# Kernel tuning notes

Hardware: AMD Instinct MI355X
Metric: run time of the kernel (lower is better)

The kernel has to match this reference:

```python
import jax, jax.numpy as jnp
import numpy as np

N_NODES = 40000
EMB = 256
NHEADS = 2
HEAD = EMB // NHEADS
NLAYERS = 4
NGNN = 2
LN_EPS = 1e-5
LEAKY = 0.01


def setup_inputs() -> dict:
    key = jax.random.key(0)
    ks = iter(jax.random.split(key, 40))
    nrm = lambda shape, s=0.05: jax.random.normal(next(ks), shape, dtype=jnp.float32) * s
    inp = {
        'feat0': nrm((20000, 512), 1.0),
        'feat1': nrm((20000, 512), 1.0),
        'fc_w0': nrm((256, 512)), 'fc_b0': jnp.zeros((256,), jnp.float32),
        'fc_w1': nrm((256, 512)), 'fc_b1': jnp.zeros((256,), jnp.float32),
        'gcn_w': nrm((NGNN, 256, 256)),
        'edge_src': jax.random.randint(next(ks), (640000,), 0, N_NODES),
        'edge_dst': jax.random.randint(next(ks), (640000,), 0, N_NODES),
        'dg_seqs': jax.random.randint(next(ks), (1024, 64), 0, N_NODES),
        'pt_seqs': jax.random.randint(next(ks), (1024, 64), 0, N_NODES),
        'type_emb': nrm((4, 4), 1.0),
        'node_type': jax.random.randint(next(ks), (N_NODES,), 0, 4),
        'gt_wl': nrm((8, 256, 256)), 'gt_wr': nrm((8, 256, 256)),
        'gt_al': nrm((8, 1, HEAD)), 'gt_ar': nrm((8, 1, HEAD)),
        'gt_wf': nrm((8, 256, 256)),
        'ln_g': jnp.ones((8, 256), jnp.float32), 'ln_b': jnp.zeros((8, 256), jnp.float32),
        'proj_d_w': nrm((2, 256, 256)), 'proj_d_b': jnp.zeros((2, 256), jnp.float32),
        'proj_p_w': nrm((2, 256, 256)), 'proj_p_b': jnp.zeros((2, 256), jnp.float32),
        'ml_w1': nrm((256, 512)), 'ml_b1': jnp.zeros((256,), jnp.float32),
        'ml_w2': nrm((128, 256)), 'ml_b2': jnp.zeros((128,), jnp.float32),
        'ml_w3': nrm((1, 128)), 'ml_b3': jnp.zeros((1,), jnp.float32),
    }
    return inp


def _layernorm(x, g, b):
    m = x.mean(-1, keepdims=True)
    v = ((x - m) ** 2).mean(-1, keepdims=True)
    return (x - m) * jax.lax.rsqrt(v + LN_EPS) * g + b


def _leaky(x):
    return jnp.where(x >= 0, x, LEAKY * x)


def _agt_layer(h, wl, wr, al, ar, wf, g, b):
    # h: [B, L, EMB]; additive (GAT-style) attention, temper = 1.0
    B, L, _ = h.shape
    fl = (h @ wl.T).reshape(B, L, NHEADS, HEAD).transpose(0, 2, 1, 3)  # [B,H,L,hd]
    fr = (h @ wr.T).reshape(B, L, NHEADS, HEAD).transpose(0, 2, 1, 3)
    sl = _leaky(fl) @ al.T                     # [B,H,L,1]
    sr = _leaky(fr) @ ar.T                     # [B,H,L,1]
    score = jax.nn.softmax(sl + sr.transpose(0, 1, 3, 2), axis=-1)  # [B,H,L,L]
    ctx = score @ fr                           # [B,H,L,hd]
    h_sa = ctx.transpose(0, 2, 1, 3).reshape(B, L, EMB)
    return _layernorm(h + h_sa @ wf.T, g, b)


def _gcn(gh, W, src, dst):
    # DGL GraphConv norm='both', allow_zero_in_degree, activation=relu
    ones = jnp.ones(src.shape[0], gh.dtype)
    deg_out = jnp.clip(jax.ops.segment_sum(ones, src, num_segments=N_NODES), 1.0)
    deg_in = jnp.clip(jax.ops.segment_sum(ones, dst, num_segments=N_NODES), 1.0)
    x = gh * (deg_out ** -0.5)[:, None]
    x = x @ W
    agg = jax.ops.segment_sum(x[src], dst, num_segments=N_NODES)
    return jax.nn.relu(agg * (deg_in ** -0.5)[:, None])


def reference(feat0, feat1, fc_w0, fc_b0, fc_w1, fc_b1, gcn_w, edge_src, edge_dst,
              dg_seqs, pt_seqs, type_emb, node_type, gt_wl, gt_wr, gt_al, gt_ar,
              gt_wf, ln_g, ln_b, proj_d_w, proj_d_b, proj_p_w, proj_p_b,
              ml_w1, ml_b1, ml_w2, ml_b2, ml_w3, ml_b3):
    # per-type input projections, concatenated along node dim
    h0 = feat0 @ fc_w0.T + fc_b0
    h1 = feat1 @ fc_w1.T + fc_b1
    gh = jnp.concatenate([h0, h1], axis=0)  # [N, EMB]
    r = type_emb[node_type]                 # computed but unused downstream (faithful)
    for layer in range(NGNN):
        gh = _gcn(gh, gcn_w[layer], edge_src, edge_dst)
    # graph transformer per node type (dropout = identity in eval)
    embs = []
    for t, seqs in ((0, dg_seqs), (1, pt_seqs)):
        h = gh[seqs]                        # [B, L, EMB]
        _ = r[seqs]
        for l in range(NLAYERS):
            i = t * NLAYERS + l
            h = _agt_layer(h, gt_wl[i], gt_wr[i], gt_al[i], gt_ar[i], gt_wf[i], ln_g[i], ln_b[i])
        embs.append(h[:, 0, :])
    dg_emb, pt_emb = embs
    # Proj heads: linear -> elu -> linear
    dg_emb = jax.nn.elu(dg_emb @ proj_d_w[0].T + proj_d_b[0]) @ proj_d_w[1].T + proj_d_b[1]
    pt_emb = jax.nn.elu(pt_emb @ proj_p_w[0].T + proj_p_b[0]) @ proj_p_w[1].T + proj_p_b[1]
    # Predict MLP on concat
    x = jnp.concatenate([dg_emb, pt_emb], axis=1)  # [B, 512]
    x = jax.nn.relu(x @ ml_w1.T + ml_b1)
    x = jax.nn.relu(x @ ml_w2.T + ml_b2)
    out = jax.nn.sigmoid(x @ ml_w3.T + ml_b3)
    return out.reshape(x.shape[0])
```

## Files before the change

### kernel.cpp

```cpp
#include <hip/hip_runtime.h>
#include <hip/hip_bf16.h>
#include <math.h>

typedef unsigned int u32;
typedef unsigned short u16;
typedef __attribute__((ext_vector_type(8))) short bf16x8;
typedef __attribute__((ext_vector_type(4))) float f32x4;

__device__ __forceinline__ float b2f(u16 u) { union { u32 i; float f; } c; c.i = ((u32)u) << 16; return c.f; }
__device__ __forceinline__ u16 f2b(float f) { __hip_bfloat16 h = __float2bfloat16(f); u16 r; __builtin_memcpy(&r, &h, 2); return r; }
__device__ __forceinline__ float b2f_lo(u32 w) { union { u32 i; float f; } c; c.i = w << 16; return c.f; }
__device__ __forceinline__ float b2f_hi(u32 w) { union { u32 i; float f; } c; c.i = w & 0xffff0000u; return c.f; }
__device__ __forceinline__ u32 pk2(float a, float b) { return (u32)f2b(a) | ((u32)f2b(b) << 16); }

__device__ __forceinline__ float wave_sum(float v) {
    #pragma unroll
    for (int off = 32; off > 0; off >>= 1) v += __shfl_xor(v, off, 64);
    return v;
}
__device__ __forceinline__ float wave_max(float v) {
    #pragma unroll
    for (int off = 32; off > 0; off >>= 1) v = fmaxf(v, __shfl_xor(v, off, 64));
    return v;
}

template<bool AF32>
__global__ __launch_bounds__(512) void mfma_gemm_kernel(
    const void* __restrict__ Av, const u16* __restrict__ B,
    const float* __restrict__ bias, const float* __restrict__ rowscale,
    u16* __restrict__ Cb, int M, int N, int K,
    const void* __restrict__ Av1, const u16* __restrict__ B1,
    const float* __restrict__ bias1, u16* __restrict__ Cb1)
{
    if (blockIdx.z) { Av = Av1; B = B1; bias = bias1; Cb = Cb1; }
    __shared__ u16 lds[2 * 128 * 64];
    const int tid = threadIdx.x;
    const int wid = tid >> 6, lane = tid & 63;
    const int wr = wid >> 1, wc = wid & 1;
    const int m0 = blockIdx.y * 128, n0 = blockIdx.x * 128;

    f32x4 acc[2][4] = {};

    const int rsub = lane >> 3;
    const int cbyte = (lane & 7) << 4;
    const int swz_st = cbyte ^ (rsub << 4);

    for (int k0 = 0; k0 < K; k0 += 64) {
        #pragma unroll
        for (int cc = 0; cc < 4; ++cc) {
            int c = wid * 4 + cc;
            int buf = c >> 4;
            int row_in = ((c & 15) << 3) + rsub;
            int lim = buf ? N : M;
            int row_g = (buf ? n0 : m0) + row_in;
            if (row_g >= lim) row_g = lim - 1;
            if (buf == 0 && AF32) {
                const float* src = (const float*)Av + (size_t)row_g * K + k0 + (cbyte >> 1);
                float4 v0 = *(const float4*)src;
                float4 v1 = *(const float4*)(src + 4);
                uint4 pk;
                pk.x = pk2(v0.x, v0.y); pk.y = pk2(v0.z, v0.w);
                pk.z = pk2(v1.x, v1.y); pk.w = pk2(v1.z, v1.w);
                *(uint4*)((char*)lds + row_in * 128 + swz_st) = pk;
            } else {
                const u16* srcb = (buf ? B : (const u16*)Av) + (size_t)row_g * K + k0 + (cbyte >> 1);
                f32x4 v = *(const f32x4*)srcb;
                *(f32x4*)((char*)lds + buf * 16384 + row_in * 128 + swz_st) = v;
            }
        }
        __syncthreads();
        #pragma unroll
        for (int ks = 0; ks < 2; ++ks) {
            const int off = (ks * 64 + ((lane >> 4) << 4)) ^ ((lane & 7) << 4);
            const int ra = lane & 15;
            bf16x8 af[2], bfr[4];
            #pragma unroll
            for (int i = 0; i < 2; ++i)
                af[i] = *(bf16x8*)((char*)lds + (wr * 32 + i * 16 + ra) * 128 + off);
            #pragma unroll
            for (int j = 0; j < 4; ++j)
                bfr[j] = *(bf16x8*)((char*)lds + 16384 + (wc * 64 + j * 16 + ra) * 128 + off);
            #pragma unroll
            for (int i = 0; i < 2; ++i)
                #pragma unroll
                for (int j = 0; j < 4; ++j)
                    acc[i][j] = __builtin_amdgcn_mfma_f32_16x16x32_bf16(af[i], bfr[j], acc[i][j], 0, 0, 0);
        }
        __syncthreads();
    }

    const int cr = lane >> 4, ccol = lane & 15;
    #pragma unroll
    for (int i = 0; i < 2; ++i) {
        #pragma unroll
        for (int j = 0; j < 4; ++j) {
            int colg = n0 + wc * 64 + j * 16 + ccol;
            if (colg >= N) continue;
            float badd = bias ? bias[colg] : 0.f;
            #pragma unroll
            for (int reg = 0; reg < 4; ++reg) {
                int rowg = m0 + wr * 32 + i * 16 + cr * 4 + reg;
                if (rowg >= M) continue;
                float v = acc[i][j][reg] + badd;
                if (rowscale) v *= rowscale[rowg];
                Cb[(size_t)rowg * N + colg] = f2b(v);
            }
        }
    }
}

__global__ __launch_bounds__(512, 4) void fused_transformer_kernel(
    const float* __restrict__ gh, const int* __restrict__ dg_seqs,
    const int* __restrict__ pt_seqs,
    const u16* __restrict__ wrN,
    const u32* __restrict__ wfT2,
    const float* __restrict__ ar,
    const float* __restrict__ lng, const float* __restrict__ lnb,
    float* __restrict__ embT)
{
    __shared__ u16 ldsA[64 * 256];
    __shared__ float sPart[8][64];
    __shared__ float pbuf[2][64];
    __shared__ float ctxS[256];
    __shared__ float uS2[2][256];

    const int tid = threadIdx.x;
    const int bx = blockIdx.x;
    const int t = bx >> 10, s = bx & 1023;
    const int r = tid >> 3, o8 = tid & 7;
    const int wid = tid >> 6, lane = tid & 63;
    const int hd = wid >> 2;
    const int g4 = lane >> 4, cl = lane & 15;

    const int* seqs = t ? pt_seqs : dg_seqs;

    float4 y[8];
    {
        int node = seqs[s * 64 + r];
        const float* src = gh + (size_t)node * 256 + o8 * 32;
        #pragma unroll
        for (int v = 0; v < 8; ++v) y[v] = *(const float4*)(src + v * 4);
    }

    for (int l = 0; l < 4; ++l) {
        const int li = t * 4 + l;
        {
            const int c = o8 >> 1, gb = (o8 & 1) * 4;
            #pragma unroll
            for (int gg = 0; gg < 4; ++gg) {
                float4 a = y[2 * gg], b = y[2 * gg + 1];
                uint4 pk;
                pk.x = pk2(a.x, a.y); pk.y = pk2(a.z, a.w);
                pk.z = pk2(b.x, b.y); pk.w = pk2(b.z, b.w);
                int g = gb + gg;
                *(uint4*)((char*)ldsA + c * 8192 + r * 128 + ((g << 4) ^ ((r & 7) << 4))) = pk;
            }
        }
        __syncthreads();

        f32x4 acc[4][2] = {};
        {
            const u16* wrl = wrN + (size_t)li * 65536;
            const int ra = lane & 15;
            #pragma unroll
            for (int kc = 0; kc < 8; ++kc) {
                const int c = kc >> 1, ks = kc & 1;
                const int off = (ks * 64 + ((lane >> 4) << 4)) ^ ((lane & 7) << 4);
                bf16x8 af[4], bfr[2];
                #pragma unroll
                for (int i = 0; i < 4; ++i)
                    af[i] = *(bf16x8*)((char*)ldsA + c * 8192 + (i * 16 + ra) * 128 + off);
                #pragma unroll
                for (int j = 0; j < 2; ++j)
                    bfr[j] = *(const bf16x8*)(wrl + ((size_t)((wid * 2 + j) * 8 + kc) << 9) + lane * 8);
                #pragma unroll
                for (int i = 0; i < 4; ++i)
                    #pragma unroll
                    for (int j = 0; j < 2; ++j)
                        acc[i][j] = __builtin_amdgcn_mfma_f32_16x16x32_bf16(af[i], bfr[j], acc[i][j], 0, 0, 0);
            }
        }

        {
            const float* arl = ar + li * 128;
            float arj[2];
            #pragma unroll
            for (int j = 0; j < 2; ++j) arj[j] = arl[(wid & 3) * 32 + j * 16 + cl];
            #pragma unroll
            for (int i = 0; i < 4; ++i)
                #pragma unroll
                for (int reg = 0; reg < 4; ++reg) {
                    float sc;
                    {
                        float x0 = acc[i][0][reg], x1 = acc[i][1][reg];
                        sc = (x0 >= 0.f ? x0 : 0.01f * x0) * arj[0]
                           + (x1 >= 0.f ? x1 : 0.01f * x1) * arj[1];
                    }
                    sc += __shfl_xor(sc, 1, 64);
                    sc += __shfl_xor(sc, 2, 64);
                    sc += __shfl_xor(sc, 4, 64);
                    sc += __shfl_xor(sc, 8, 64);
                    if (cl == 0) sPart[wid][i * 16 + g4 * 4 + reg] = sc;
                }
        }
        __syncthreads();

        {
            int base = hd * 4;
            float sv = sPart[base][lane] + sPart[base + 1][lane]
                     + sPart[base + 2][lane] + sPart[base + 3][lane];
            float mx = wave_max(sv);
            float e = expf(sv - mx);
            float sm = wave_sum(e);
            if ((wid & 3) == 0) pbuf[hd][lane] = e / sm;
        }
        __syncthreads();

        {
            float pv[4][4];
            #pragma unroll
            for (int i = 0; i < 4; ++i)
                #pragma unroll
                for (int reg = 0; reg < 4; ++reg)
                    pv[i][reg] = pbuf[hd][i * 16 + g4 * 4 + reg];
            #pragma unroll
            for (int j = 0; j < 2; ++j) {
                float c = 0.f;
                #pragma unroll
                for (int i = 0; i < 4; ++i)
                    #pragma unroll
                    for (int reg = 0; reg < 4; ++reg)
                        c = fmaf(pv[i][reg], acc[i][j][reg], c);
                c += __shfl_xor(c, 16, 64);
                c += __shfl_xor(c, 32, 64);
                if (g4 == 0) ctxS[wid * 32 + j * 16 + cl] = c;
            }
        }
        __syncthreads();

        {
            const int n = tid & 255, half = tid >> 8;
            const u32* wp = wfT2 + (size_t)li * 32768 + (size_t)half * 16384 + n;
            float ua = 0.f;
            #pragma unroll 8
            for (int d2 = 0; d2 < 64; ++d2) {
                u32 w2 = wp[(size_t)d2 * 256];
                ua = fmaf(ctxS[half * 128 + 2 * d2], b2f_lo(w2), ua);
                ua = fmaf(ctxS[half * 128 + 2 * d2 + 1], b2f_hi(w2), ua);
            }
            uS2[half][n] = ua;
        }
        __syncthreads();

        {
            #pragma unroll
            for (int v = 0; v < 8; ++v) {
                int c0 = o8 * 32 + v * 4;
                float4 u0 = *(const float4*)&uS2[0][c0];
                float4 u1 = *(const float4*)&uS2[1][c0];
                y[v].x += u0.x + u1.x; y[v].y += u0.y + u1.y;
                y[v].z += u0.z + u1.z; y[v].w += u0.w + u1.w;
            }
            float sm = 0.f, qq = 0.f;
            #pragma unroll
            for (int v = 0; v < 8; ++v) {
                sm += y[v].x + y[v].y + y[v].z + y[v].w;
                qq += y[v].x * y[v].x + y[v].y * y[v].y + y[v].z * y[v].z + y[v].w * y[v].w;
            }
            sm += __shfl_xor(sm, 1, 64); sm += __shfl_xor(sm, 2, 64); sm += __shfl_xor(sm, 4, 64);
            qq += __shfl_xor(qq, 1, 64); qq += __shfl_xor(qq, 2, 64); qq += __shfl_xor(qq, 4, 64);
            float mean = sm * (1.f / 256.f);
            float var = qq * (1.f / 256.f) - mean * mean;
            float inv = rsqrtf(var + 1e-5f);
            const float* gl = lng + li * 256 + o8 * 32;
            const float* bl = lnb + li * 256 + o8 * 32;
            if (l < 3) {
                #pragma unroll
                for (int v = 0; v < 8; ++v) {
                    float4 gv = *(const float4*)(gl + v * 4);
                    float4 bv = *(const float4*)(bl + v * 4);
                    y[v].x = (y[v].x - mean) * inv * gv.x + bv.x;
                    y[v].y = (y[v].y - mean) * inv * gv.y + bv.y;
                    y[v].z = (y[v].z - mean) * inv * gv.z + bv.z;
                    y[v].w = (y[v].w - mean) * inv * gv.w + bv.w;
                }
            } else if (r == 0) {
                float* dst = embT + (size_t)(t * 1024 + s) * 256 + o8 * 32;
                #pragma unroll
                for (int v = 0; v < 8; ++v) {
                    float4 gv = *(const float4*)(gl + v * 4);
                    float4 bv = *(const float4*)(bl + v * 4);
                    float4 o;
                    o.x = (y[v].x - mean) * inv * gv.x + bv.x;
                    o.y = (y[v].y - mean) * inv * gv.y + bv.y;
                    o.z = (y[v].z - mean) * inv * gv.z + bv.z;
                    o.w = (y[v].w - mean) * inv * gv.w + bv.w;
                    *(float4*)(dst + v * 4) = o;
                }
            }
        }
        __syncthreads();
    }
}

template<bool BT>
__global__ __launch_bounds__(256) void gemm_kernel(
    const float* __restrict__ A, const float* __restrict__ B,
    const float* __restrict__ bias, const float* __restrict__ rowscale,
    float* __restrict__ C,
    int M, int N, int K, int lda, int ldb, int ldc, int coff, int act)
{
    __shared__ float As[32][64 + 4];
    __shared__ float Bs[32][64 + 4];
    const int tid = threadIdx.x;
    const int m0 = blockIdx.y * 64;
    const int n0 = blockIdx.x * 64;
    const int ty = tid >> 4, tx = tid & 15;
    float acc[4][4] = {};
    for (int k0 = 0; k0 < K; k0 += 32) {
        #pragma unroll
        for (int r = 0; r < 2; ++r) {
            int f4 = tid + r * 256;
            int arw = f4 >> 3, af = (f4 & 7) << 2;
            float4 v = make_float4(0.f, 0.f, 0.f, 0.f);
            int grow = m0 + arw;
            if (grow < M) {
                v = *(const float4*)(A + (size_t)grow * lda + k0 + af);
                if (rowscale) { float s = rowscale[grow]; v.x *= s; v.y *= s; v.z *= s; v.w *= s; }
            }
            As[af + 0][arw] = v.x; As[af + 1][arw] = v.y; As[af + 2][arw] = v.z; As[af + 3][arw] = v.w;
        }
        #pragma unroll
        for (int r = 0; r < 2; ++r) {
            int f4 = tid + r * 256;
            int col = f4 >> 3, kf = (f4 & 7) << 2;
            float4 v = make_float4(0.f, 0.f, 0.f, 0.f);
            if (n0 + col < N) v = *(const float4*)(B + (size_t)(n0 + col) * ldb + k0 + kf);
            Bs[kf + 0][col] = v.x; Bs[kf + 1][col] = v.y; Bs[kf + 2][col] = v.z; Bs[kf + 3][col] = v.w;
        }
        __syncthreads();
        #pragma unroll
        for (int kk = 0; kk < 32; ++kk) {
            float4 a4 = *(const float4*)&As[kk][ty << 2];
            float4 b4 = *(const float4*)&Bs[kk][tx << 2];
            float a[4] = {a4.x, a4.y, a4.z, a4.w};
            float b[4] = {b4.x, b4.y, b4.z, b4.w};
            #pragma unroll
            for (int i = 0; i < 4; ++i)
                #pragma unroll
                for (int j = 0; j < 4; ++j)
                    acc[i][j] = fmaf(a[i], b[j], acc[i][j]);
        }
        __syncthreads();
    }
    #pragma unroll
    for (int i = 0; i < 4; ++i) {
        int row = m0 + (ty << 2) + i;
        if (row >= M) continue;
        #pragma unroll
        for (int j = 0; j < 4; ++j) {
            int col = n0 + (tx << 2) + j;
            if (col >= N) continue;
            float v = acc[i][j];
            if (bias) v += bias[col];
            if (act == 1) v = fmaxf(v, 0.f);
            else if (act == 2) v = (v > 0.f) ? v : expm1f(v);
            C[(size_t)row * ldc + coff + col] = v;
        }
    }
}

__global__ __launch_bounds__(256) void conv_flat_kernel(const float* __restrict__ in, u16* __restrict__ out, int n) {
    int i = (blockIdx.x * 256 + threadIdx.x) * 4;
    if (i >= n) return;
    float4 v = *(const float4*)(in + i);
    *(uint2*)(out + i) = make_uint2(pk2(v.x, v.y), pk2(v.z, v.w));
}
__global__ __launch_bounds__(256) void conv_gcnw_kernel(const float* __restrict__ w, u16* __restrict__ out) {
    int idx = blockIdx.x * 256 + threadIdx.x;
    int l = blockIdx.y;
    int k = idx >> 8, n = idx & 255;
    out[(size_t)l * 65536 + n * 256 + k] = f2b(w[(size_t)l * 65536 + k * 256 + n]);
}
__global__ __launch_bounds__(256) void conv_wrN_kernel(const float* __restrict__ w, u16* __restrict__ out) {
    int idx = blockIdx.x * 256 + threadIdx.x;
    int lane = idx & 63;
    int kc = (idx >> 6) & 7;
    int gn = (idx >> 9) & 15;
    int l = idx >> 13;
    int row = gn * 16 + (lane & 15);
    int k0 = kc * 32 + (lane >> 4) * 8;
    const float* src = w + ((size_t)l * 256 + row) * 256 + k0;
    float4 v0 = *(const float4*)src;
    float4 v1 = *(const float4*)(src + 4);
    uint4 pk;
    pk.x = pk2(v0.x, v0.y); pk.y = pk2(v0.z, v0.w);
    pk.z = pk2(v1.x, v1.y); pk.w = pk2(v1.z, v1.w);
    *(uint4*)(out + (size_t)idx * 8) = pk;
}
__global__ __launch_bounds__(256) void conv_wfT2_kernel(const float* __restrict__ w, u32* __restrict__ out) {
    int idx = blockIdx.x * 256 + threadIdx.x;
    int n = idx & 255;
    int d2 = (idx >> 8) & 127;
    int l = idx >> 15;
    const float* src = w + ((size_t)l * 256 + n) * 256 + 2 * d2;
    out[idx] = pk2(src[0], src[1]);
}

#define EDGE_CAP 128
__global__ __launch_bounds__(256) void bucket_fill_kernel(
    const int* __restrict__ src, const int* __restrict__ dst,
    int* __restrict__ ebuf, int* __restrict__ cursor, int* __restrict__ cnt_out, int ne)
{
    int e = blockIdx.x * 256 + threadIdx.x;
    if (e >= ne) return;
    int s = src[e], d = dst[e];
    atomicAdd(&cnt_out[s], 1);
    int pos = atomicAdd(&cursor[d], 1);
    if (pos < EDGE_CAP) ebuf[(size_t)d * EDGE_CAP + pos] = s;
}
__global__ __launch_bounds__(256) void deg_fin_kernel(const int* __restrict__ cnt, float* __restrict__ dinv, int n) {
    int i = blockIdx.x * 256 + threadIdx.x;
    if (i < n) dinv[i] = rsqrtf(fmaxf((float)cnt[i], 1.0f));
}

__global__ __launch_bounds__(256) void csr_agg_kernel(
    const u16* __restrict__ x, const int* __restrict__ ebuf,
    const int* __restrict__ deg, float* __restrict__ outf, u16* __restrict__ outb, int nnodes)
{
    int n = blockIdx.x * 4 + (threadIdx.x >> 6);
    if (n >= nnodes) return;
    int lane = threadIdx.x & 63;
    int d = deg[n];
    float dinv = rsqrtf(fmaxf((float)d, 1.0f));
    if (d > EDGE_CAP) d = EDGE_CAP;
    const int* eb = ebuf + (size_t)n * EDGE_CAP;
    const int co = lane << 2;
    float a0 = 0.f, a1 = 0.f, a2 = 0.f, a3 = 0.f;
    int k = 0;
    for (; k + 4 <= d; k += 4) {
        int4 s4 = *(const int4*)(eb + k);
        uint2 va = *(const uint2*)(x + (size_t)s4.x * 256 + co);
        uint2 vb = *(const uint2*)(x + (size_t)s4.y * 256 + co);
        uint2 vc = *(const uint2*)(x + (size_t)s4.z * 256 + co);
        uint2 vd = *(const uint2*)(x + (size_t)s4.w * 256 + co);
        a0 += b2f_lo(va.x) + b2f_lo(vb.x) + b2f_lo(vc.x) + b2f_lo(vd.x);
        a1 += b2f_hi(va.x) + b2f_hi(vb.x) + b2f_hi(vc.x) + b2f_hi(vd.x);
        a2 += b2f_lo(va.y) + b2f_lo(vb.y) + b2f_lo(vc.y) + b2f_lo(vd.y);
        a3 += b2f_hi(va.y) + b2f_hi(vb.y) + b2f_hi(vc.y) + b2f_hi(vd.y);
    }
    for (; k < d; ++k) {
        int s = eb[k];
        uint2 v = *(const uint2*)(x + (size_t)s * 256 + co);
        a0 += b2f_lo(v.x); a1 += b2f_hi(v.x);
        a2 += b2f_lo(v.y); a3 += b2f_hi(v.y);
    }
    a0 = fmaxf(a0 * dinv, 0.f); a1 = fmaxf(a1 * dinv, 0.f);
    a2 = fmaxf(a2 * dinv, 0.f); a3 = fmaxf(a3 * dinv, 0.f);
    *(float4*)(outf + (size_t)n * 256 + co) = make_float4(a0, a1, a2, a3);
    *(uint2*)(outb + (size_t)n * 256 + co) = make_uint2(pk2(a0, a1), pk2(a2, a3));
}

__global__ __launch_bounds__(256) void final_kernel(
    const float* __restrict__ m2, const float* __restrict__ w3,
    const float* __restrict__ b3, float* __restrict__ out, int nrows)
{
    int row = blockIdx.x * 4 + (threadIdx.x >> 6);
    int lane = threadIdx.x & 63;
    if (row >= nrows) return;
    float s = m2[(size_t)row * 128 + lane] * w3[lane]
            + m2[(size_t)row * 128 + 64 + lane] * w3[64 + lane];
    s = wave_sum(s);
    if (lane == 0) out[row] = 1.f / (1.f + expf(-(s + b3[0])));
}

static inline int cdiv(int a, int b) { return (a + b - 1) / b; }

extern "C" void kernel_launch(void* const* d_in, const int* in_sizes, int n_in,
                              void* d_out, int out_size, void* d_ws, size_t ws_size,
                              hipStream_t stream)
{
    const float* feat0   = (const float*)d_in[0];
    const float* feat1   = (const float*)d_in[1];
    const float* fc_w0   = (const float*)d_in[2];
    const float* fc_b0   = (const float*)d_in[3];
    const float* fc_w1   = (const float*)d_in[4];
    const float* fc_b1   = (const float*)d_in[5];
    const float* gcn_w   = (const float*)d_in[6];
    const int*   edge_src= (const int*)d_in[7];
    const int*   edge_dst= (const int*)d_in[8];
    const int*   dg_seqs = (const int*)d_in[9];
    const int*   pt_seqs = (const int*)d_in[10];
    const float* gt_wr   = (const float*)d_in[14];
    const float* gt_ar   = (const float*)d_in[16];
    const float* gt_wf   = (const float*)d_in[17];
    const float* ln_g    = (const float*)d_in[18];
    const float* ln_b    = (const float*)d_in[19];
    const float* proj_d_w= (const float*)d_in[20];
    const float* proj_d_b= (const float*)d_in[21];
    const float* proj_p_w= (const float*)d_in[22];
    const float* proj_p_b= (const float*)d_in[23];
    const float* ml_w1   = (const float*)d_in[24];
    const float* ml_b1   = (const float*)d_in[25];
    const float* ml_w2   = (const float*)d_in[26];
    const float* ml_b2   = (const float*)d_in[27];
    const float* ml_w3   = (const float*)d_in[28];
    const float* ml_b3   = (const float*)d_in[29];
    float* out = (float*)d_out;

    float* base  = (float*)d_ws;
    float* gh    = base;
    float* gcnR  = gh + 10240000;
    float* dego  = gcnR + 15440000;
    float* embT  = dego + 40000;
    float* t1    = embT + 524288;
    float* mx    = t1 + 262144;
    float* m1    = mx + 524288;
    float* m2    = m1 + 262144;
    float* wreg  = m2 + 131072;

    u16* tmp_b   = (u16*)gcnR;
    int* ebuf    = (int*)(gcnR + 5120000);
    int* cursor  = ebuf + (size_t)40000 * EDGE_CAP;
    int* cnt_out = cursor + 40000;
    u16* gh_b    = (u16*)(gcnR + 10320000);

    u16* fcw_b   = (u16*)wreg;
    u16* gcnw_b  = fcw_b + 262144;
    u16* wrN     = gcnw_b + 131072;
    u32* wfT2    = (u32*)(wrN + 524288);

    conv_flat_kernel<<<cdiv(131072 / 4, 256), 256, 0, stream>>>(fc_w0, fcw_b, 131072);
    conv_flat_kernel<<<cdiv(131072 / 4, 256), 256, 0, stream>>>(fc_w1, fcw_b + 131072, 131072);
    conv_gcnw_kernel<<<dim3(256, 2), 256, 0, stream>>>(gcn_w, gcnw_b);
    conv_wrN_kernel<<<256, 256, 0, stream>>>(gt_wr, wrN);
    conv_wfT2_kernel<<<1024, 256, 0, stream>>>(gt_wf, wfT2);

    mfma_gemm_kernel<true><<<dim3(2, cdiv(20000, 128), 2), 512, 0, stream>>>(
        feat0, fcw_b, fc_b0, nullptr, gh_b, 20000, 256, 512,
        feat1, fcw_b + 131072, fc_b1, gh_b + (size_t)20000 * 256);

    hipMemsetAsync(cursor, 0, 80000 * sizeof(int), stream);
    bucket_fill_kernel<<<2500, 256, 0, stream>>>(edge_src, edge_dst, ebuf, cursor, cnt_out, 640000);
    deg_fin_kernel<<<cdiv(40000, 256), 256, 0, stream>>>(cnt_out, dego, 40000);

    for (int l = 0; l < 2; ++l) {
        mfma_gemm_kernel<false><<<dim3(2, cdiv(40000, 128), 1), 512, 0, stream>>>(
            gh_b, gcnw_b + (size_t)l * 65536, nullptr, dego, tmp_b, 40000, 256, 256,
            gh_b, gcnw_b, nullptr, tmp_b);
        csr_agg_kernel<<<10000, 256, 0, stream>>>(tmp_b, ebuf, cursor, gh, gh_b, 40000);
    }

    fused_transformer_kernel<<<2048, 512, 0, stream>>>(
        gh, dg_seqs, pt_seqs, wrN, wfT2, gt_ar, ln_g, ln_b, embT);

    const float* pw[2] = {proj_d_w, proj_p_w};
    const float* pb[2] = {proj_d_b, proj_p_b};
    for (int t = 0; t < 2; ++t) {
        gemm_kernel<true><<<dim3(4, 16), 256, 0, stream>>>(
            embT + (size_t)t * 262144, pw[t], pb[t], nullptr, t1, 1024, 256, 256, 256, 256, 256, 0, 2);
        gemm_kernel<true><<<dim3(4, 16), 256, 0, stream>>>(
            t1, pw[t] + 65536, pb[t] + 256, nullptr, mx, 1024, 256, 256, 256, 256, 512, t * 256, 0);
    }

    gemm_kernel<true><<<dim3(4, 16), 256, 0, stream>>>(
        mx, ml_w1, ml_b1, nullptr, m1, 1024, 256, 512, 512, 512, 256, 0, 1);
    gemm_kernel<true><<<dim3(2, 16), 256, 0, stream>>>(
        m1, ml_w2, ml_b2, nullptr, m2, 1024, 128, 256, 256, 256, 128, 0, 1);
    final_kernel<<<256, 256, 0, stream>>>(m2, ml_w3, ml_b3, out, 1024);
}
```

Baseline: 708.7 us.

## Shrink GEMM tiles, alias transformer LDS, batch head GEMMs, vectorize bucket fill

Result: no change. 695.5 us (-1.9%).

```diff
diff --git a/kernel.cpp b/kernel.cpp
--- a/kernel.cpp
+++ b/kernel.cpp
@@ -25,7 +25,7 @@
 }
 
 template<bool AF32>
-__global__ __launch_bounds__(512) void mfma_gemm_kernel(
+__global__ __launch_bounds__(256) void mfma_gemm_kernel(
     const void* __restrict__ Av, const u16* __restrict__ B,
     const float* __restrict__ bias, const float* __restrict__ rowscale,
     u16* __restrict__ Cb, int M, int N, int K,
@@ -33,40 +33,41 @@
     const float* __restrict__ bias1, u16* __restrict__ Cb1)
 {
     if (blockIdx.z) { Av = Av1; B = B1; bias = bias1; Cb = Cb1; }
-    __shared__ u16 lds[2 * 128 * 64];
+    __shared__ u16 lds[(64 + 128) * 64];
     const int tid = threadIdx.x;
     const int wid = tid >> 6, lane = tid & 63;
     const int wr = wid >> 1, wc = wid & 1;
-    const int m0 = blockIdx.y * 128, n0 = blockIdx.x * 128;
+    const int m0 = blockIdx.y * 64, n0 = blockIdx.x * 128;
 
     f32x4 acc[2][4] = {};
 
-    const int rsub = lane >> 3;
-    const int cbyte = (lane & 7) << 4;
-    const int swz_st = cbyte ^ (rsub << 4);
-
     for (int k0 = 0; k0 < K; k0 += 64) {
         #pragma unroll
-        for (int cc = 0; cc < 4; ++cc) {
-            int c = wid * 4 + cc;
-            int buf = c >> 4;
-            int row_in = ((c & 15) << 3) + rsub;
-            int lim = buf ? N : M;
-            int row_g = (buf ? n0 : m0) + row_in;
-            if (row_g >= lim) row_g = lim - 1;
-            if (buf == 0 && AF32) {
-                const float* src = (const float*)Av + (size_t)row_g * K + k0 + (cbyte >> 1);
+        for (int s = 0; s < 2; ++s) {
+            int idx = tid + s * 256;
+            int row = idx >> 3, g = idx & 7;
+            int row_g = m0 + row; if (row_g >= M) row_g = M - 1;
+            int swz = ((g << 4) ^ ((row & 7) << 4));
+            if (AF32) {
+                const float* src = (const float*)Av + (size_t)row_g * K + k0 + g * 8;
                 float4 v0 = *(const float4*)src;
                 float4 v1 = *(const float4*)(src + 4);
                 uint4 pk;
                 pk.x = pk2(v0.x, v0.y); pk.y = pk2(v0.z, v0.w);
                 pk.z = pk2(v1.x, v1.y); pk.w = pk2(v1.z, v1.w);
-                *(uint4*)((char*)lds + row_in * 128 + swz_st) = pk;
+                *(uint4*)((char*)lds + row * 128 + swz) = pk;
             } else {
-                const u16* srcb = (buf ? B : (const u16*)Av) + (size_t)row_g * K + k0 + (cbyte >> 1);
-                f32x4 v = *(const f32x4*)srcb;
-                *(f32x4*)((char*)lds + buf * 16384 + row_in * 128 + swz_st) = v;
-            }
+                f32x4 v = *(const f32x4*)((const u16*)Av + (size_t)row_g * K + k0 + g * 8);
+                *(f32x4*)((char*)lds + row * 128 + swz) = v;
+            }
+        }
+        #pragma unroll
+        for (int s = 0; s < 4; ++s) {
+            int idx = tid + s * 256;
+            int row = idx >> 3, g = idx & 7;
+            int row_g = n0 + row; if (row_g >= N) row_g = N - 1;
+            f32x4 v = *(const f32x4*)(B + (size_t)row_g * K + k0 + g * 8);
+            *(f32x4*)((char*)lds + 8192 + row * 128 + ((g << 4) ^ ((row & 7) << 4))) = v;
         }
         __syncthreads();
         #pragma unroll
@@ -79,7 +80,7 @@
                 af[i] = *(bf16x8*)((char*)lds + (wr * 32 + i * 16 + ra) * 128 + off);
             #pragma unroll
             for (int j = 0; j < 4; ++j)
-                bfr[j] = *(bf16x8*)((char*)lds + 16384 + (wc * 64 + j * 16 + ra) * 128 + off);
+                bfr[j] = *(bf16x8*)((char*)lds + 8192 + (wc * 64 + j * 16 + ra) * 128 + off);
             #pragma unroll
             for (int i = 0; i < 2; ++i)
                 #pragma unroll
@@ -119,10 +120,10 @@
     float* __restrict__ embT)
 {
     __shared__ u16 ldsA[64 * 256];
-    __shared__ float sPart[8][64];
-    __shared__ float pbuf[2][64];
-    __shared__ float ctxS[256];
-    __shared__ float uS2[2][256];
+    float* sPartO = (float*)ldsA;
+    float* pbufO  = sPartO + 512;
+    float* ctxO   = pbufO + 128;
+    float* uO     = ctxO + 256;
 
     const int tid = threadIdx.x;
     const int bx = blockIdx.x;
@@ -180,6 +181,7 @@
                         acc[i][j] = __builtin_amdgcn_mfma_f32_16x16x32_bf16(af[i], bfr[j], acc[i][j], 0, 0, 0);
             }
         }
+        __syncthreads();
 
         {
             const float* arl = ar + li * 128;
@@ -200,19 +202,19 @@
                     sc += __shfl_xor(sc, 2, 64);
                     sc += __shfl_xor(sc, 4, 64);
                     sc += __shfl_xor(sc, 8, 64);
-                    if (cl == 0) sPart[wid][i * 16 + g4 * 4 + reg] = sc;
+                    if (cl == 0) sPartO[wid * 64 + i * 16 + g4 * 4 + reg] = sc;
                 }
         }
         __syncthreads();
 
         {
-            int base = hd * 4;
-            float sv = sPart[base][lane] + sPart[base + 1][lane]
-                     + sPart[base + 2][lane] + sPart[base + 3][lane];
+            int base = hd * 4 * 64;
+            float sv = sPartO[base + lane] + sPartO[base + 64 + lane]
+                     + sPartO[base + 128 + lane] + sPartO[base + 192 + lane];
             float mx = wave_max(sv);
             float e = expf(sv - mx);
             float sm = wave_sum(e);
-            if ((wid & 3) == 0) pbuf[hd][lane] = e / sm;
+            if ((wid & 3) == 0) pbufO[hd * 64 + lane] = e / sm;
         }
         __syncthreads();
 
@@ -222,7 +224,7 @@
             for (int i = 0; i < 4; ++i)
                 #pragma unroll
                 for (int reg = 0; reg < 4; ++reg)
-                    pv[i][reg] = pbuf[hd][i * 16 + g4 * 4 + reg];
+                    pv[i][reg] = pbufO[hd * 64 + i * 16 + g4 * 4 + reg];
             #pragma unroll
             for (int j = 0; j < 2; ++j) {
                 float c = 0.f;
@@ -233,7 +235,7 @@
                         c = fmaf(pv[i][reg], acc[i][j][reg], c);
                 c += __shfl_xor(c, 16, 64);
                 c += __shfl_xor(c, 32, 64);
-                if (g4 == 0) ctxS[wid * 32 + j * 16 + cl] = c;
+                if (g4 == 0) ctxO[wid * 32 + j * 16 + cl] = c;
             }
         }
         __syncthreads();
@@ -241,14 +243,24 @@
         {
             const int n = tid & 255, half = tid >> 8;
             const u32* wp = wfT2 + (size_t)li * 32768 + (size_t)half * 16384 + n;
-            float ua = 0.f;
-            #pragma unroll 8
-            for (int d2 = 0; d2 < 64; ++d2) {
-                u32 w2 = wp[(size_t)d2 * 256];
-                ua = fmaf(ctxS[half * 128 + 2 * d2], b2f_lo(w2), ua);
-                ua = fmaf(ctxS[half * 128 + 2 * d2 + 1], b2f_hi(w2), ua);
-            }
-            uS2[half][n] = ua;
+            const float* cx = ctxO + half * 128;
+            float ua0 = 0.f, ua1 = 0.f, ua2 = 0.f, ua3 = 0.f;
+            #pragma unroll 4
+            for (int d2 = 0; d2 < 64; d2 += 4) {
+                u32 w0 = wp[(size_t)(d2 + 0) * 256];
+                u32 w1 = wp[(size_t)(d2 + 1) * 256];
+                u32 w2 = wp[(size_t)(d2 + 2) * 256];
+                u32 w3 = wp[(size_t)(d2 + 3) * 256];
+                ua0 = fmaf(cx[2 * d2 + 0], b2f_lo(w0), ua0);
+                ua0 = fmaf(cx[2 * d2 + 1], b2f_hi(w0), ua0);
+                ua1 = fmaf(cx[2 * d2 + 2], b2f_lo(w1), ua1);
+                ua1 = fmaf(cx[2 * d2 + 3], b2f_hi(w1), ua1);
+                ua2 = fmaf(cx[2 * d2 + 4], b2f_lo(w2), ua2);
+                ua2 = fmaf(cx[2 * d2 + 5], b2f_hi(w2), ua2);
+                ua3 = fmaf(cx[2 * d2 + 6], b2f_lo(w3), ua3);
+                ua3 = fmaf(cx[2 * d2 + 7], b2f_hi(w3), ua3);
+            }
+            uO[half * 256 + n] = (ua0 + ua1) + (ua2 + ua3);
         }
         __syncthreads();
 
@@ -256,8 +268,8 @@
             #pragma unroll
             for (int v = 0; v < 8; ++v) {
                 int c0 = o8 * 32 + v * 4;
-                float4 u0 = *(const float4*)&uS2[0][c0];
-                float4 u1 = *(const float4*)&uS2[1][c0];
+                float4 u0 = *(const float4*)&uO[c0];
+                float4 u1 = *(const float4*)&uO[256 + c0];
                 y[v].x += u0.x + u1.x; y[v].y += u0.y + u1.y;
                 y[v].z += u0.z + u1.z; y[v].w += u0.w + u1.w;
             }
@@ -308,8 +320,11 @@
     const float* __restrict__ A, const float* __restrict__ B,
     const float* __restrict__ bias, const float* __restrict__ rowscale,
     float* __restrict__ C,
-    int M, int N, int K, int lda, int ldb, int ldc, int coff, int act)
-{
+    int M, int N, int K, int lda, int ldb, int ldc, int coff, int act,
+    const float* __restrict__ A1, const float* __restrict__ B1,
+    const float* __restrict__ bias1, float* __restrict__ C1, int coff1)
+{
+    if (blockIdx.z) { A = A1; B = B1; bias = bias1; C = C1; coff = coff1; }
     __shared__ float As[32][64 + 4];
     __shared__ float Bs[32][64 + 4];
     const int tid = threadIdx.x;
@@ -412,12 +427,22 @@
     const int* __restrict__ src, const int* __restrict__ dst,
     int* __restrict__ ebuf, int* __restrict__ cursor, int* __restrict__ cnt_out, int ne)
 {
-    int e = blockIdx.x * 256 + threadIdx.x;
-    if (e >= ne) return;
-    int s = src[e], d = dst[e];
-    atomicAdd(&cnt_out[s], 1);
-    int pos = atomicAdd(&cursor[d], 1);
-    if (pos < EDGE_CAP) ebuf[(size_t)d * EDGE_CAP + pos] = s;
+    int e0 = (blockIdx.x * 256 + threadIdx.x) * 4;
+    if (e0 >= ne) return;
+    int4 s4 = *(const int4*)(src + e0);
+    int4 d4 = *(const int4*)(dst + e0);
+    atomicAdd(&cnt_out[s4.x], 1);
+    atomicAdd(&cnt_out[s4.y], 1);
+    atomicAdd(&cnt_out[s4.z], 1);
+    atomicAdd(&cnt_out[s4.w], 1);
+    int p0 = atomicAdd(&cursor[d4.x], 1);
+    int p1 = atomicAdd(&cursor[d4.y], 1);
+    int p2 = atomicAdd(&cursor[d4.z], 1);
+    int p3 = atomicAdd(&cursor[d4.w], 1);
+    if (p0 < EDGE_CAP) ebuf[(size_t)d4.x * EDGE_CAP + p0] = s4.x;
+    if (p1 < EDGE_CAP) ebuf[(size_t)d4.y * EDGE_CAP + p1] = s4.y;
+    if (p2 < EDGE_CAP) ebuf[(size_t)d4.z * EDGE_CAP + p2] = s4.z;
+    if (p3 < EDGE_CAP) ebuf[(size_t)d4.w * EDGE_CAP + p3] = s4.w;
 }
 __global__ __launch_bounds__(256) void deg_fin_kernel(const int* __restrict__ cnt, float* __restrict__ dinv, int n) {
     int i = blockIdx.x * 256 + threadIdx.x;
@@ -514,7 +539,7 @@
     float* dego  = gcnR + 15440000;
     float* embT  = dego + 40000;
     float* t1    = embT + 524288;
-    float* mx    = t1 + 262144;
+    float* mx    = t1 + 524288;
     float* m1    = mx + 524288;
     float* m2    = m1 + 262144;
     float* wreg  = m2 + 131072;
@@ -536,16 +561,16 @@
     conv_wrN_kernel<<<256, 256, 0, stream>>>(gt_wr, wrN);
     conv_wfT2_kernel<<<1024, 256, 0, stream>>>(gt_wf, wfT2);
 
-    mfma_gemm_kernel<true><<<dim3(2, cdiv(20000, 128), 2), 512, 0, stream>>>(
+    mfma_gemm_kernel<true><<<dim3(2, cdiv(20000, 64), 2), 256, 0, stream>>>(
         feat0, fcw_b, fc_b0, nullptr, gh_b, 20000, 256, 512,
         feat1, fcw_b + 131072, fc_b1, gh_b + (size_t)20000 * 256);
 
     hipMemsetAsync(cursor, 0, 80000 * sizeof(int), stream);
-    bucket_fill_kernel<<<2500, 256, 0, stream>>>(edge_src, edge_dst, ebuf, cursor, cnt_out, 640000);
+    bucket_fill_kernel<<<625, 256, 0, stream>>>(edge_src, edge_dst, ebuf, cursor, cnt_out, 640000);
     deg_fin_kernel<<<cdiv(40000, 256), 256, 0, stream>>>(cnt_out, dego, 40000);
 
     for (int l = 0; l < 2; ++l) {
-        mfma_gemm_kernel<false><<<dim3(2, cdiv(40000, 128), 1), 512, 0, stream>>>(
+        mfma_gemm_kernel<false><<<dim3(2, cdiv(40000, 64), 1), 256, 0, stream>>>(
             gh_b, gcnw_b + (size_t)l * 65536, nullptr, dego, tmp_b, 40000, 256, 256,
             gh_b, gcnw_b, nullptr, tmp_b);
         csr_agg_kernel<<<10000, 256, 0, stream>>>(tmp_b, ebuf, cursor, gh, gh_b, 40000);
@@ -554,18 +579,18 @@
     fused_transformer_kernel<<<2048, 512, 0, stream>>>(
         gh, dg_seqs, pt_seqs, wrN, wfT2, gt_ar, ln_g, ln_b, embT);
 
-    const float* pw[2] = {proj_d_w, proj_p_w};
-    const float* pb[2] = {proj_d_b, proj_p_b};
-    for (int t = 0; t < 2; ++t) {
-        gemm_kernel<true><<<dim3(4, 16), 256, 0, stream>>>(
-            embT + (size_t)t * 262144, pw[t], pb[t], nullptr, t1, 1024, 256, 256, 256, 256, 256, 0, 2);
-        gemm_kernel<true><<<dim3(4, 16), 256, 0, stream>>>(
-            t1, pw[t] + 65536, pb[t] + 256, nullptr, mx, 1024, 256, 256, 256, 256, 512, t * 256, 0);
-    }
-
-    gemm_kernel<true><<<dim3(4, 16), 256, 0, stream>>>(
-        mx, ml_w1, ml_b1, nullptr, m1, 1024, 256, 512, 512, 512, 256, 0, 1);
-    gemm_kernel<true><<<dim3(2, 16), 256, 0, stream>>>(
-        m1, ml_w2, ml_b2, nullptr, m2, 1024, 128, 256, 256, 256, 128, 0, 1);
+    gemm_kernel<true><<<dim3(4, 16, 2), 256, 0, stream>>>(
+        embT, proj_d_w, proj_d_b, nullptr, t1, 1024, 256, 256, 256, 256, 256, 0, 2,
+        embT + 262144, proj_p_w, proj_p_b, t1 + 262144, 0);
+    gemm_kernel<true><<<dim3(4, 16, 2), 256, 0, stream>>>(
+        t1, proj_d_w + 65536, proj_d_b + 256, nullptr, mx, 1024, 256, 256, 256, 256, 512, 0, 0,
+        t1 + 262144, proj_p_w + 65536, proj_p_b + 256, mx, 256);
+
+    gemm_kernel<true><<<dim3(4, 16, 1), 256, 0, stream>>>(
+        mx, ml_w1, ml_b1, nullptr, m1, 1024, 256, 512, 512, 512, 256, 0, 1,
+        mx, ml_w1, ml_b1, m1, 0);
+    gemm_kernel<true><<<dim3(2, 16, 1), 256, 0, stream>>>(
+        m1, ml_w2, ml_b2, nullptr, m2, 1024, 128, 256, 256, 256, 128, 0, 1,
+        m1, ml_w2, ml_b2, m2, 0);
     final_kernel<<<256, 256, 0, stream>>>(m2, ml_w3, ml_b3, out, 1024);
 }
```
